# Optimization experiments

Measured on AMD Instinct MI355X. Metric: run time of the kernel, lower is better.

The kernel has to match this reference:

```python
import jax, jax.numpy as jnp
import numpy as np

CONF_THRESH = 0.01
TOP_K = 200
NMS_THRESH = 0.45


def setup_inputs() -> dict:
    key = jax.random.key(0)
    k1, k2, k3, k4, k5 = jax.random.split(key, 5)
    B, N, C = 32, 8732, 21
    return {
        "loc_data": jax.random.normal(k1, (B, N, 4), jnp.float32),
        "conf_data": jax.random.normal(k2, (B, N, C), jnp.float32),
        "pose_data": jax.random.normal(k3, (B, N, 32), jnp.float32),
        "line_data": jax.random.normal(k4, (B, N, 3), jnp.float32),
        "dbox_list": jax.random.uniform(k5, (N, 4), jnp.float32),
    }


def decode(loc, dbox):
    # loc, dbox: [N,4]; variances 0.1 / 0.2 as in the torch decode()
    cxcy = dbox[:, :2] + loc[:, :2] * 0.1 * dbox[:, 2:]
    wh = dbox[:, 2:] * jnp.exp(loc[:, 2:] * 0.2)
    mins = cxcy - wh / 2.0
    maxs = mins + wh
    return jnp.concatenate([mins, maxs], axis=1)  # [N,4] xyxy


def nms_class(boxes, scores, poses, lines):
    """Greedy NMS for one (batch, class). boxes [N,4], scores [N] (softmax probs).
    Matches torch nm_suppression: candidates are the top_k by score above
    conf_thresh; suppress IoU > overlap; at most top_k kept."""
    s0 = jnp.where(scores > CONF_THRESH, scores, -jnp.inf)
    _, cand_idx = jax.lax.top_k(s0, TOP_K)  # descending-score candidate pool
    cb = boxes[cand_idx]                     # [K,4]
    cs = s0[cand_idx]                        # [K], -inf where below threshold
    x1, y1, x2, y2 = cb[:, 0], cb[:, 1], cb[:, 2], cb[:, 3]
    area = (x2 - x1) * (y2 - y1)
    K = TOP_K
    ar = jnp.arange(K)

    def step(s, _):
        i = jnp.argmax(s)
        take = jnp.isfinite(s[i])
        xx1 = jnp.maximum(x1, x1[i])
        yy1 = jnp.maximum(y1, y1[i])
        xx2 = jnp.minimum(x2, x2[i])
        yy2 = jnp.minimum(y2, y2[i])
        inter = jnp.clip(xx2 - xx1, 0.0) * jnp.clip(yy2 - yy1, 0.0)
        union = area - inter + area[i]
        iou = inter / union
        supp = (iou > NMS_THRESH) | (ar == i)
        s_new = jnp.where(take & supp, -jnp.inf, s)
        return s_new, (i, take)

    _, (pos, take) = jax.lax.scan(step, cs, None, length=K)
    gi = cand_idx[pos]  # global box indices of kept detections [K]
    row = jnp.concatenate(
        [scores[gi][:, None], boxes[gi], poses[gi], lines[gi]], axis=1
    )  # [K, 1+4+32+3] = [200, 40]
    return row * take[:, None].astype(row.dtype)


def reference(loc_data, conf_data, pose_data, line_data, dbox_list):
    conf = jax.nn.softmax(conf_data, axis=-1)                       # [B,N,C]
    boxes = jax.vmap(decode, in_axes=(0, None))(loc_data, dbox_list)  # [B,N,4]
    per_cls = jax.vmap(nms_class, in_axes=(None, 1, None, None))    # over classes
    per_batch = jax.vmap(per_cls, in_axes=(0, 0, 0, 0))             # over batch
    out = per_batch(boxes, conf, pose_data, line_data)              # [B,C,200,40]
    return out.at[:, 0].set(0.0)  # class 0 (background) is skipped in torch loop
```

## Files before the change

### kernel.cpp

```cpp
#include <hip/hip_runtime.h>
#include <math.h>

#define BB 32
#define NN 8732
#define CC 21
#define TOPK 200
#define NPOSE 32
#define NLINE 3
#define NBINS 2048
#define CAP 1024
#define ROWW 40

__device__ __forceinline__ double fexp(double x) {
  const double LOG2E = 1.4426950408889634074;
  const double LN2HI = 6.93147180369123816490e-01;
  const double LN2LO = 1.90821492927058770002e-10;
  double kd = rint(x * LOG2E);
  double r = fma(-kd, LN2HI, x);
  r = fma(-kd, LN2LO, r);
  double p = 2.08767569878680989792e-09;
  p = fma(p, r, 2.50521083854417187751e-08);
  p = fma(p, r, 2.75573192239858906526e-07);
  p = fma(p, r, 2.75573192239858925110e-06);
  p = fma(p, r, 2.48015873015873015873e-05);
  p = fma(p, r, 1.98412698412698412698e-04);
  p = fma(p, r, 1.38888888888888888889e-03);
  p = fma(p, r, 8.33333333333333333333e-03);
  p = fma(p, r, 4.16666666666666666667e-02);
  p = fma(p, r, 1.66666666666666666667e-01);
  p = fma(p, r, 0.5);
  p = fma(p, r, 1.0);
  p = fma(p, r, 1.0);
  int k = (int)kd;
  k = k < -1020 ? -1020 : (k > 1020 ? 1020 : k);
  double sc = __longlong_as_double((long long)(1023 + k) << 52);
  return p * sc;
}

__global__ __launch_bounds__(256, 4) void score_kernel(
    const float* __restrict__ conf, float* __restrict__ scores) {
  __shared__ __align__(16) float buf[256 * CC];
  const int tid = threadIdx.x;
  const int i0 = blockIdx.x * 256;
  const int base = i0 * CC;
  int total = BB * NN * CC - base;
  if (total > 256 * CC) total = 256 * CC;
  {
    const float4* g4 = (const float4*)(conf + base);
    float4* b4 = (float4*)buf;
    const int n4 = total >> 2;
    for (int t = tid; t < n4; t += 256) b4[t] = g4[t];
  }
  __syncthreads();
  const int i = i0 + tid;
  if (i >= BB * NN) return;
  const float* p = buf + tid * CC;
  float x[CC];
#pragma unroll
  for (int c = 0; c < CC; ++c) x[c] = p[c];
  float m = x[0];
#pragma unroll
  for (int c = 1; c < CC; ++c) m = fmaxf(m, x[c]);
  float e[CC];
#pragma unroll
  for (int c = 0; c < CC; ++c) e[c] = (float)fexp((double)(x[c] - m));
  float r0 = e[0] + e[8], r1 = e[1] + e[9], r2 = e[2] + e[10], r3 = e[3] + e[11];
  float r4 = e[4] + e[12], r5 = e[5] + e[13], r6 = e[6] + e[14], r7 = e[7] + e[15];
  float sum = ((r0 + r1) + (r2 + r3)) + ((r4 + r5) + (r6 + r7));
  sum += e[16]; sum += e[17]; sum += e[18]; sum += e[19]; sum += e[20];
  const int b = i / NN, n = i - b * NN;
#pragma unroll
  for (int c = 0; c < CC; ++c)
    scores[((size_t)b * CC + c) * NN + n] = e[c] / sum;
}

__global__ __launch_bounds__(256) void aux_kernel(
    const float* __restrict__ conf, float2* __restrict__ aux) {
  int i = blockIdx.x * 256 + threadIdx.x;
  if (i >= BB * NN) return;
  const float* p = conf + (size_t)i * CC;
  float m = p[0];
#pragma unroll
  for (int c = 1; c < CC; ++c) m = fmaxf(m, p[c]);
  float e[CC];
#pragma unroll 1
  for (int c = 0; c < CC; ++c) e[c] = (float)fexp((double)(p[c] - m));
  float r0 = e[0] + e[8], r1 = e[1] + e[9], r2 = e[2] + e[10], r3 = e[3] + e[11];
  float r4 = e[4] + e[12], r5 = e[5] + e[13], r6 = e[6] + e[14], r7 = e[7] + e[15];
  float sum = ((r0 + r1) + (r2 + r3)) + ((r4 + r5) + (r6 + r7));
  sum += e[16]; sum += e[17]; sum += e[18]; sum += e[19]; sum += e[20];
  aux[i] = make_float2(m, sum);
}

__device__ __forceinline__ int score_bin(float s) {
  unsigned u = __float_as_uint(s);
  int bin = (int)(u >> 15) - 30720;
  return bin < 0 ? 0 : (bin > NBINS - 1 ? NBINS - 1 : bin);
}

__device__ __forceinline__ float score_at(int mode, int b, int c, int n,
                                          const float* conf, const float2* auxB,
                                          const float* confB) {
  if (mode == 1) {
    float2 a = auxB[n];
    return (float)fexp((double)(confB[(size_t)n * CC] - a.x)) / a.y;
  }
  const float* p = conf + ((size_t)b * NN + n) * CC;
  float mm = p[0];
  for (int c2 = 1; c2 < CC; ++c2) mm = fmaxf(mm, p[c2]);
  float e[CC];
  for (int c2 = 0; c2 < CC; ++c2) e[c2] = (float)fexp((double)(p[c2] - mm));
  float r0 = e[0] + e[8], r1 = e[1] + e[9], r2 = e[2] + e[10], r3 = e[3] + e[11];
  float r4 = e[4] + e[12], r5 = e[5] + e[13], r6 = e[6] + e[14], r7 = e[7] + e[15];
  float sum = ((r0 + r1) + (r2 + r3)) + ((r4 + r5) + (r6 + r7));
  sum += e[16]; sum += e[17]; sum += e[18]; sum += e[19]; sum += e[20];
  return e[c] / sum;
}

__global__ __launch_bounds__(256) void nms_kernel(
    const float* __restrict__ loc, const float* __restrict__ conf,
    const float* __restrict__ pose, const float* __restrict__ line,
    const float* __restrict__ dbox, const float* __restrict__ scores,
    const float2* __restrict__ aux, int mode, float* __restrict__ out) {
  const int bc = blockIdx.x;
  const int b = bc / CC, c = bc - b * CC;
  const int tid = threadIdx.x;
  const int wv = tid >> 6, lane = tid & 63;
  float* outSlab = out + (size_t)bc * (TOPK * ROWW);
  const float4 z4 = make_float4(0.f, 0.f, 0.f, 0.f);

  if (c == 0) {
    float4* o4 = (float4*)outSlab;
    for (int i = tid; i < TOPK * ROWW / 4; i += 256) o4[i] = z4;
    return;
  }

  __shared__ int hist[NBINS];
  __shared__ float cscore[CAP];
  __shared__ int cidx[CAP];
  __shared__ float bx1[TOPK], by1[TOPK], bx2[TOPK], by2[TOPK], barea[TOPK];
  __shared__ unsigned long long supp[TOPK * 4];
  __shared__ int kept[TOPK];
  __shared__ int waveTot[4];
  __shared__ int sBT, sCnt, sKept;

  for (int i = tid; i < NBINS; i += 256) hist[i] = 0;
  if (tid == 0) { sCnt = 0; sBT = 0; }
  __syncthreads();

  const float* scoresB = scores + ((size_t)b * CC + c) * NN;
  const float2* auxB = aux + (size_t)b * NN;
  const float* confB = conf + (size_t)b * NN * CC + c;

  float4 v[9];
  if (mode == 2) {
#pragma unroll
    for (int k = 0; k < 8; ++k)
      v[k] = *(const float4*)(scoresB + k * 1024 + tid * 4);
    if (tid < 135)
      v[8] = *(const float4*)(scoresB + 8192 + tid * 4);
    else
      v[8] = make_float4(-1.f, -1.f, -1.f, -1.f);
#pragma unroll
    for (int k = 0; k < 9; ++k) {
      if (v[k].x > 0.01f) atomicAdd(&hist[score_bin(v[k].x)], 1);
      if (v[k].y > 0.01f) atomicAdd(&hist[score_bin(v[k].y)], 1);
      if (v[k].z > 0.01f) atomicAdd(&hist[score_bin(v[k].z)], 1);
      if (v[k].w > 0.01f) atomicAdd(&hist[score_bin(v[k].w)], 1);
    }
  } else {
    for (int n = tid; n < NN; n += 256) {
      float s = score_at(mode, b, c, n, conf, auxB, confB);
      if (s > 0.01f) atomicAdd(&hist[score_bin(s)], 1);
    }
  }
  __syncthreads();

  int s8 = 0;
#pragma unroll
  for (int k = 0; k < 8; ++k) s8 += hist[tid * 8 + k];
  int cs = s8;
#pragma unroll
  for (int d = 1; d < 64; d <<= 1) {
    int t = __shfl_down(cs, d, 64);
    if (lane + d < 64) cs += t;
  }
  if (lane == 0) waveTot[wv] = cs;
  __syncthreads();
  {
    int higher = 0;
    for (int g = wv + 1; g < 4; ++g) higher += waveTot[g];
    int incl = cs + higher;
    int excl = incl - s8;
    if (excl < TOPK && incl >= TOPK) {
      int cum = excl, bt = tid * 8;
      for (int bin = tid * 8 + 7;; --bin) {
        cum += hist[bin];
        if (cum >= TOPK || bin == tid * 8) { bt = bin; break; }
      }
      sBT = bt;
    }
  }
  __syncthreads();
  const int bt = sBT;

  if (mode == 2) {
#pragma unroll
    for (int k = 0; k < 9; ++k) {
      float sv[4] = {v[k].x, v[k].y, v[k].z, v[k].w};
#pragma unroll
      for (int j = 0; j < 4; ++j) {
        float s = sv[j];
        if (s > 0.01f && score_bin(s) >= bt) {
          int p = atomicAdd(&sCnt, 1);
          if (p < CAP) { cscore[p] = s; cidx[p] = k * 1024 + tid * 4 + j; }
        }
      }
    }
  } else {
    for (int n = tid; n < NN; n += 256) {
      float s = score_at(mode, b, c, n, conf, auxB, confB);
      if (s > 0.01f && score_bin(s) >= bt) {
        int p = atomicAdd(&sCnt, 1);
        if (p < CAP) { cscore[p] = s; cidx[p] = n; }
      }
    }
  }
  __syncthreads();
  const int M = sCnt < CAP ? sCnt : CAP;
  if (M == 0) {
    float4* o4 = (float4*)outSlab;
    for (int i = tid; i < TOPK * ROWW / 4; i += 256) o4[i] = z4;
    return;
  }

  int P = 1;
  while (P < M) P <<= 1;
  for (int i = M + tid; i < P; i += 256) {
    cscore[i] = -1e30f;
    cidx[i] = 0x7fffffff;
  }
  __syncthreads();
  for (int k = 2; k <= P; k <<= 1) {
    for (int j = k >> 1; j > 0; j >>= 1) {
      for (int i = tid; i < P; i += 256) {
        int ixj = i ^ j;
        if (ixj > i) {
          float si = cscore[i], sj = cscore[ixj];
          int ii = cidx[i], ij = cidx[ixj];
          bool agt = (si > sj) || (si == sj && ii < ij);
          bool up = ((i & k) == 0);
          if (up ? !agt : agt) {
            cscore[i] = sj; cscore[ixj] = si;
            cidx[i] = ij;  cidx[ixj] = ii;
          }
        }
      }
      __syncthreads();
    }
  }

  const int K = M < TOPK ? M : TOPK;

  const float* locB = loc + (size_t)b * NN * 4;
  for (int t = tid; t < K; t += 256) {
    int n = cidx[t];
    float l0 = locB[(size_t)n * 4 + 0], l1 = locB[(size_t)n * 4 + 1];
    float l2 = locB[(size_t)n * 4 + 2], l3 = locB[(size_t)n * 4 + 3];
    float d0 = dbox[(size_t)n * 4 + 0], d1 = dbox[(size_t)n * 4 + 1];
    float d2 = dbox[(size_t)n * 4 + 2], d3 = dbox[(size_t)n * 4 + 3];
    float cx = d0 + (l0 * 0.1f) * d2;
    float cy = d1 + (l1 * 0.1f) * d3;
    float w = d2 * (float)fexp((double)(l2 * 0.2f));
    float h = d3 * (float)fexp((double)(l3 * 0.2f));
    float x1 = cx - w * 0.5f;
    float y1 = cy - h * 0.5f;
    float x2 = x1 + w;
    float y2 = y1 + h;
    bx1[t] = x1; by1[t] = y1; bx2[t] = x2; by2[t] = y2;
    barea[t] = (x2 - x1) * (y2 - y1);
  }
  __syncthreads();

  {
    const int l = wv * 64 + lane;
    float lx1 = 0.f, ly1 = 0.f, lx2 = 0.f, ly2 = 0.f, lar = 0.f;
    const bool lvalid = l < K;
    if (lvalid) { lx1 = bx1[l]; ly1 = by1[l]; lx2 = bx2[l]; ly2 = by2[l]; lar = barea[l]; }
    const int wtop = wv * 64 + 63;
    for (int j = 0; j < K; ++j) {
      unsigned long long mres = 0;
      if (wtop > j) {
        float jx1 = bx1[j], jy1 = by1[j], jx2 = bx2[j], jy2 = by2[j], ja = barea[j];
        float xx1 = fmaxf(lx1, jx1);
        float yy1 = fmaxf(ly1, jy1);
        float xx2 = fminf(lx2, jx2);
        float yy2 = fminf(ly2, jy2);
        float iw = fmaxf(xx2 - xx1, 0.0f);
        float ih = fmaxf(yy2 - yy1, 0.0f);
        float inter = iw * ih;
        float uni = (lar - inter) + ja;
        bool hit = lvalid & (l > j) & (inter / uni > 0.45f);
        mres = __ballot((int)hit);
      }
      if (lane == 0) supp[j * 4 + wv] = mres;
    }
  }
  __syncthreads();

  if (tid == 0) {
    unsigned long long alive[4];
#pragma unroll
    for (int w = 0; w < 4; ++w) {
      int cnt = K - w * 64;
      alive[w] = cnt <= 0 ? 0ull : (cnt >= 64 ? ~0ull : ((1ull << cnt) - 1ull));
    }
    int nk = 0;
#pragma unroll
    for (int w = 0; w < 4; ++w) {
      while (alive[w]) {
        int bit = __ffsll(alive[w]) - 1;
        int j = w * 64 + bit;
        kept[nk++] = j;
        unsigned long long r0 = supp[j * 4 + 0];
        unsigned long long r1 = supp[j * 4 + 1];
        unsigned long long r2 = supp[j * 4 + 2];
        unsigned long long r3 = supp[j * 4 + 3];
        alive[w] &= ~(1ull << bit);
        alive[0] &= ~r0; alive[1] &= ~r1; alive[2] &= ~r2; alive[3] &= ~r3;
      }
    }
    sKept = nk;
  }
  __syncthreads();

  const int nk = sKept;
  const float* poseB = pose + (size_t)b * NN * NPOSE;
  const float* lineB = line + (size_t)b * NN * NLINE;
  for (int t = tid; t < nk; t += 256) {
    int j = kept[t];
    int n = cidx[j];
    float* row = outSlab + (size_t)t * ROWW;
    row[0] = cscore[j];
    row[1] = bx1[j];
    row[2] = by1[j];
    row[3] = bx2[j];
    row[4] = by2[j];
    const float4* p4 = (const float4*)(poseB + (size_t)n * NPOSE);
#pragma unroll
    for (int q = 0; q < 8; ++q) {
      float4 pv = p4[q];
      row[5 + 4 * q + 0] = pv.x;
      row[5 + 4 * q + 1] = pv.y;
      row[5 + 4 * q + 2] = pv.z;
      row[5 + 4 * q + 3] = pv.w;
    }
    row[37] = lineB[(size_t)n * NLINE + 0];
    row[38] = lineB[(size_t)n * NLINE + 1];
    row[39] = lineB[(size_t)n * NLINE + 2];
  }
  {
    const int zq = (TOPK - nk) * 10;
    float4* o4 = (float4*)(outSlab + (size_t)nk * ROWW);
    for (int q = tid; q < zq; q += 256) o4[q] = z4;
  }
}

extern "C" void kernel_launch(void* const* d_in, const int* in_sizes, int n_in,
                              void* d_out, int out_size, void* d_ws, size_t ws_size,
                              hipStream_t stream) {
  const float* loc  = (const float*)d_in[0];
  const float* conf = (const float*)d_in[1];
  const float* pose = (const float*)d_in[2];
  const float* line = (const float*)d_in[3];
  const float* dbox = (const float*)d_in[4];
  float* out = (float*)d_out;

  const size_t scoreBytes = (size_t)BB * CC * NN * sizeof(float);
  const size_t auxBytes   = (size_t)BB * NN * sizeof(float2);

  int mode;
  float* scores = nullptr;
  float2* aux = nullptr;
  if (ws_size >= scoreBytes) {
    mode = 2; scores = (float*)d_ws;
  } else if (ws_size >= auxBytes) {
    mode = 1; aux = (float2*)d_ws;
  } else {
    mode = 0;
  }

  const int total = BB * NN;
  if (mode == 2) {
    score_kernel<<<(total + 255) / 256, 256, 0, stream>>>(conf, scores);
  } else if (mode == 1) {
    aux_kernel<<<(total + 255) / 256, 256, 0, stream>>>(conf, aux);
  }
  nms_kernel<<<BB * CC, 256, 0, stream>>>(loc, conf, pose, line, dbox,
                                          scores, aux, mode, out);
}
```

Baseline: 187.1 us.

## Replace full per-class score tensor with per-row softmax max/sum stats

The pre-pass that wrote a full transposed [B,C,N] softmax score tensor is dropped. A smem-staged kernel now writes only a per-row (max, sum) pair. The NMS kernel recomputes each class score from conf plus these stats once, keeps the scores in registers, and reuses them for both the histogram and the candidate-selection passes. The greedy NMS scan also skips reading suppression rows that are entirely zero, using a ballot-built bitmask. This cuts large workspace write/read traffic, at the cost of strided 84-byte-stride conf reads and a double-precision exp per element inside the NMS kernel.

```diff
diff --git a/kernel.cpp b/kernel.cpp
--- a/kernel.cpp
+++ b/kernel.cpp
@@ -37,8 +37,8 @@
   return p * sc;
 }
 
-__global__ __launch_bounds__(256, 4) void score_kernel(
-    const float* __restrict__ conf, float* __restrict__ scores) {
+__global__ __launch_bounds__(256) void aux_kernel(
+    const float* __restrict__ conf, float2* __restrict__ aux) {
   __shared__ __align__(16) float buf[256 * CC];
   const int tid = threadIdx.x;
   const int i0 = blockIdx.x * 256;
@@ -55,30 +55,6 @@
   const int i = i0 + tid;
   if (i >= BB * NN) return;
   const float* p = buf + tid * CC;
-  float x[CC];
-#pragma unroll
-  for (int c = 0; c < CC; ++c) x[c] = p[c];
-  float m = x[0];
-#pragma unroll
-  for (int c = 1; c < CC; ++c) m = fmaxf(m, x[c]);
-  float e[CC];
-#pragma unroll
-  for (int c = 0; c < CC; ++c) e[c] = (float)fexp((double)(x[c] - m));
-  float r0 = e[0] + e[8], r1 = e[1] + e[9], r2 = e[2] + e[10], r3 = e[3] + e[11];
-  float r4 = e[4] + e[12], r5 = e[5] + e[13], r6 = e[6] + e[14], r7 = e[7] + e[15];
-  float sum = ((r0 + r1) + (r2 + r3)) + ((r4 + r5) + (r6 + r7));
-  sum += e[16]; sum += e[17]; sum += e[18]; sum += e[19]; sum += e[20];
-  const int b = i / NN, n = i - b * NN;
-#pragma unroll
-  for (int c = 0; c < CC; ++c)
-    scores[((size_t)b * CC + c) * NN + n] = e[c] / sum;
-}
-
-__global__ __launch_bounds__(256) void aux_kernel(
-    const float* __restrict__ conf, float2* __restrict__ aux) {
-  int i = blockIdx.x * 256 + threadIdx.x;
-  if (i >= BB * NN) return;
-  const float* p = conf + (size_t)i * CC;
   float m = p[0];
 #pragma unroll
   for (int c = 1; c < CC; ++c) m = fmaxf(m, p[c]);
@@ -98,13 +74,7 @@
   return bin < 0 ? 0 : (bin > NBINS - 1 ? NBINS - 1 : bin);
 }
 
-__device__ __forceinline__ float score_at(int mode, int b, int c, int n,
-                                          const float* conf, const float2* auxB,
-                                          const float* confB) {
-  if (mode == 1) {
-    float2 a = auxB[n];
-    return (float)fexp((double)(confB[(size_t)n * CC] - a.x)) / a.y;
-  }
+__device__ __forceinline__ float score_full(const float* conf, int b, int c, int n) {
   const float* p = conf + ((size_t)b * NN + n) * CC;
   float mm = p[0];
   for (int c2 = 1; c2 < CC; ++c2) mm = fmaxf(mm, p[c2]);
@@ -120,8 +90,8 @@
 __global__ __launch_bounds__(256) void nms_kernel(
     const float* __restrict__ loc, const float* __restrict__ conf,
     const float* __restrict__ pose, const float* __restrict__ line,
-    const float* __restrict__ dbox, const float* __restrict__ scores,
-    const float2* __restrict__ aux, int mode, float* __restrict__ out) {
+    const float* __restrict__ dbox, const float2* __restrict__ aux,
+    int mode, float* __restrict__ out) {
   const int bc = blockIdx.x;
   const int b = bc / CC, c = bc - b * CC;
   const int tid = threadIdx.x;
@@ -140,6 +110,7 @@
   __shared__ int cidx[CAP];
   __shared__ float bx1[TOPK], by1[TOPK], bx2[TOPK], by2[TOPK], barea[TOPK];
   __shared__ unsigned long long supp[TOPK * 4];
+  __shared__ unsigned long long rowAnyBits[4];
   __shared__ int kept[TOPK];
   __shared__ int waveTot[4];
   __shared__ int sBT, sCnt, sKept;
@@ -148,31 +119,46 @@
   if (tid == 0) { sCnt = 0; sBT = 0; }
   __syncthreads();
 
-  const float* scoresB = scores + ((size_t)b * CC + c) * NN;
   const float2* auxB = aux + (size_t)b * NN;
   const float* confB = conf + (size_t)b * NN * CC + c;
 
-  float4 v[9];
-  if (mode == 2) {
-#pragma unroll
-    for (int k = 0; k < 8; ++k)
-      v[k] = *(const float4*)(scoresB + k * 1024 + tid * 4);
-    if (tid < 135)
-      v[8] = *(const float4*)(scoresB + 8192 + tid * 4);
-    else
-      v[8] = make_float4(-1.f, -1.f, -1.f, -1.f);
+  float s36[36];
+  if (mode == 1) {
 #pragma unroll
     for (int k = 0; k < 9; ++k) {
-      if (v[k].x > 0.01f) atomicAdd(&hist[score_bin(v[k].x)], 1);
-      if (v[k].y > 0.01f) atomicAdd(&hist[score_bin(v[k].y)], 1);
-      if (v[k].z > 0.01f) atomicAdd(&hist[score_bin(v[k].z)], 1);
-      if (v[k].w > 0.01f) atomicAdd(&hist[score_bin(v[k].w)], 1);
+      const int n0 = k * 1024 + (tid << 2);
+      if (k < 8 || tid < 135) {
+        float4 a01 = *(const float4*)(auxB + n0);
+        float4 a23 = *(const float4*)(auxB + n0 + 2);
+        float c0 = confB[(size_t)(n0 + 0) * CC];
+        float c1 = confB[(size_t)(n0 + 1) * CC];
+        float c2 = confB[(size_t)(n0 + 2) * CC];
+        float c3 = confB[(size_t)(n0 + 3) * CC];
+        s36[k * 4 + 0] = (float)fexp((double)(c0 - a01.x)) / a01.y;
+        s36[k * 4 + 1] = (float)fexp((double)(c1 - a01.z)) / a01.w;
+        s36[k * 4 + 2] = (float)fexp((double)(c2 - a23.x)) / a23.y;
+        s36[k * 4 + 3] = (float)fexp((double)(c3 - a23.z)) / a23.w;
+      } else {
+        s36[k * 4 + 0] = -1.f; s36[k * 4 + 1] = -1.f;
+        s36[k * 4 + 2] = -1.f; s36[k * 4 + 3] = -1.f;
+      }
     }
   } else {
-    for (int n = tid; n < NN; n += 256) {
-      float s = score_at(mode, b, c, n, conf, auxB, confB);
-      if (s > 0.01f) atomicAdd(&hist[score_bin(s)], 1);
-    }
+#pragma unroll 1
+    for (int k = 0; k < 9; ++k) {
+      const int n0 = k * 1024 + (tid << 2);
+      if (k < 8 || tid < 135) {
+        for (int q = 0; q < 4; ++q) s36[k * 4 + q] = score_full(conf, b, c, n0 + q);
+      } else {
+        for (int q = 0; q < 4; ++q) s36[k * 4 + q] = -1.f;
+      }
+    }
+  }
+
+#pragma unroll
+  for (int k2 = 0; k2 < 36; ++k2) {
+    float s = s36[k2];
+    if (s > 0.01f) atomicAdd(&hist[score_bin(s)], 1);
   }
   __syncthreads();
 
@@ -204,25 +190,14 @@
   __syncthreads();
   const int bt = sBT;
 
-  if (mode == 2) {
-#pragma unroll
-    for (int k = 0; k < 9; ++k) {
-      float sv[4] = {v[k].x, v[k].y, v[k].z, v[k].w};
-#pragma unroll
-      for (int j = 0; j < 4; ++j) {
-        float s = sv[j];
-        if (s > 0.01f && score_bin(s) >= bt) {
-          int p = atomicAdd(&sCnt, 1);
-          if (p < CAP) { cscore[p] = s; cidx[p] = k * 1024 + tid * 4 + j; }
-        }
-      }
-    }
-  } else {
-    for (int n = tid; n < NN; n += 256) {
-      float s = score_at(mode, b, c, n, conf, auxB, confB);
-      if (s > 0.01f && score_bin(s) >= bt) {
-        int p = atomicAdd(&sCnt, 1);
-        if (p < CAP) { cscore[p] = s; cidx[p] = n; }
+#pragma unroll
+  for (int k2 = 0; k2 < 36; ++k2) {
+    float s = s36[k2];
+    if (s > 0.01f && score_bin(s) >= bt) {
+      int p = atomicAdd(&sCnt, 1);
+      if (p < CAP) {
+        cscore[p] = s;
+        cidx[p] = (k2 >> 2) * 1024 + (tid << 2) + (k2 & 3);
       }
     }
   }
@@ -308,6 +283,16 @@
   }
   __syncthreads();
 
+  {
+    bool nz = false;
+    if (tid < K)
+      nz = (supp[tid * 4 + 0] | supp[tid * 4 + 1] |
+            supp[tid * 4 + 2] | supp[tid * 4 + 3]) != 0ull;
+    unsigned long long bal = __ballot((int)nz);
+    if (lane == 0) rowAnyBits[wv] = bal;
+  }
+  __syncthreads();
+
   if (tid == 0) {
     unsigned long long alive[4];
 #pragma unroll
@@ -318,16 +303,19 @@
     int nk = 0;
 #pragma unroll
     for (int w = 0; w < 4; ++w) {
+      const unsigned long long raw = rowAnyBits[w];
       while (alive[w]) {
         int bit = __ffsll(alive[w]) - 1;
         int j = w * 64 + bit;
         kept[nk++] = j;
-        unsigned long long r0 = supp[j * 4 + 0];
-        unsigned long long r1 = supp[j * 4 + 1];
-        unsigned long long r2 = supp[j * 4 + 2];
-        unsigned long long r3 = supp[j * 4 + 3];
         alive[w] &= ~(1ull << bit);
-        alive[0] &= ~r0; alive[1] &= ~r1; alive[2] &= ~r2; alive[3] &= ~r3;
+        if ((raw >> bit) & 1) {
+          unsigned long long r0 = supp[j * 4 + 0];
+          unsigned long long r1 = supp[j * 4 + 1];
+          unsigned long long r2 = supp[j * 4 + 2];
+          unsigned long long r3 = supp[j * 4 + 3];
+          alive[0] &= ~r0; alive[1] &= ~r1; alive[2] &= ~r2; alive[3] &= ~r3;
+        }
       }
     }
     sKept = nk;
@@ -376,26 +364,14 @@
   const float* dbox = (const float*)d_in[4];
   float* out = (float*)d_out;
 
-  const size_t scoreBytes = (size_t)BB * CC * NN * sizeof(float);
-  const size_t auxBytes   = (size_t)BB * NN * sizeof(float2);
-
-  int mode;
-  float* scores = nullptr;
-  float2* aux = nullptr;
-  if (ws_size >= scoreBytes) {
-    mode = 2; scores = (float*)d_ws;
-  } else if (ws_size >= auxBytes) {
-    mode = 1; aux = (float2*)d_ws;
-  } else {
-    mode = 0;
-  }
-
-  const int total = BB * NN;
-  if (mode == 2) {
-    score_kernel<<<(total + 255) / 256, 256, 0, stream>>>(conf, scores);
-  } else if (mode == 1) {
+  const size_t auxBytes = (size_t)BB * NN * sizeof(float2);
+  int mode = (ws_size >= auxBytes) ? 1 : 0;
+  float2* aux = mode ? (float2*)d_ws : nullptr;
+
+  if (mode) {
+    const int total = BB * NN;
     aux_kernel<<<(total + 255) / 256, 256, 0, stream>>>(conf, aux);
   }
   nms_kernel<<<BB * CC, 256, 0, stream>>>(loc, conf, pose, line, dbox,
-                                          scores, aux, mode, out);
-}
+                                          aux, mode, out);
+}
```

After: 231.3 us. 23.6% more time.

## Replace bitonic candidate sort with rank-by-count selection and skip empty suppression rows

Applied to the files above, without the earlier changes.

Packs each candidate's score and index into one 64-bit key and gives every candidate its final position by counting how many keys are larger. This replaces the bitonic sort that needed many barriers. Boxes are stored as float4 and loaded with vector loads. The IoU test becomes a double-precision FMA against a threshold, which avoids the divide. A bitmap of rows with any suppression lets the serial greedy pass skip supp reads for rows that suppress nothing. The aux-workspace fallback path is removed. The counting rank costs O(M^2) shared-memory reads, which may be slow when the candidate pool is large.

```diff
diff --git a/kernel.cpp b/kernel.cpp
--- a/kernel.cpp
+++ b/kernel.cpp
@@ -74,37 +74,13 @@
     scores[((size_t)b * CC + c) * NN + n] = e[c] / sum;
 }
 
-__global__ __launch_bounds__(256) void aux_kernel(
-    const float* __restrict__ conf, float2* __restrict__ aux) {
-  int i = blockIdx.x * 256 + threadIdx.x;
-  if (i >= BB * NN) return;
-  const float* p = conf + (size_t)i * CC;
-  float m = p[0];
-#pragma unroll
-  for (int c = 1; c < CC; ++c) m = fmaxf(m, p[c]);
-  float e[CC];
-#pragma unroll 1
-  for (int c = 0; c < CC; ++c) e[c] = (float)fexp((double)(p[c] - m));
-  float r0 = e[0] + e[8], r1 = e[1] + e[9], r2 = e[2] + e[10], r3 = e[3] + e[11];
-  float r4 = e[4] + e[12], r5 = e[5] + e[13], r6 = e[6] + e[14], r7 = e[7] + e[15];
-  float sum = ((r0 + r1) + (r2 + r3)) + ((r4 + r5) + (r6 + r7));
-  sum += e[16]; sum += e[17]; sum += e[18]; sum += e[19]; sum += e[20];
-  aux[i] = make_float2(m, sum);
-}
-
 __device__ __forceinline__ int score_bin(float s) {
   unsigned u = __float_as_uint(s);
   int bin = (int)(u >> 15) - 30720;
   return bin < 0 ? 0 : (bin > NBINS - 1 ? NBINS - 1 : bin);
 }
 
-__device__ __forceinline__ float score_at(int mode, int b, int c, int n,
-                                          const float* conf, const float2* auxB,
-                                          const float* confB) {
-  if (mode == 1) {
-    float2 a = auxB[n];
-    return (float)fexp((double)(confB[(size_t)n * CC] - a.x)) / a.y;
-  }
+__device__ __forceinline__ float score_full(const float* conf, int b, int c, int n) {
   const float* p = conf + ((size_t)b * NN + n) * CC;
   float mm = p[0];
   for (int c2 = 1; c2 < CC; ++c2) mm = fmaxf(mm, p[c2]);
@@ -121,7 +97,7 @@
     const float* __restrict__ loc, const float* __restrict__ conf,
     const float* __restrict__ pose, const float* __restrict__ line,
     const float* __restrict__ dbox, const float* __restrict__ scores,
-    const float2* __restrict__ aux, int mode, float* __restrict__ out) {
+    int mode, float* __restrict__ out) {
   const int bc = blockIdx.x;
   const int b = bc / CC, c = bc - b * CC;
   const int tid = threadIdx.x;
@@ -136,10 +112,13 @@
   }
 
   __shared__ int hist[NBINS];
-  __shared__ float cscore[CAP];
-  __shared__ int cidx[CAP];
-  __shared__ float bx1[TOPK], by1[TOPK], bx2[TOPK], by2[TOPK], barea[TOPK];
+  __shared__ unsigned long long ckey[CAP];
+  __shared__ float4 cbox[TOPK];
+  __shared__ float carea[TOPK];
+  __shared__ float sScore[TOPK];
+  __shared__ int sIdx[TOPK];
   __shared__ unsigned long long supp[TOPK * 4];
+  __shared__ unsigned long long rowAnyBits[4];
   __shared__ int kept[TOPK];
   __shared__ int waveTot[4];
   __shared__ int sBT, sCnt, sKept;
@@ -149,11 +128,9 @@
   __syncthreads();
 
   const float* scoresB = scores + ((size_t)b * CC + c) * NN;
-  const float2* auxB = aux + (size_t)b * NN;
-  const float* confB = conf + (size_t)b * NN * CC + c;
 
   float4 v[9];
-  if (mode == 2) {
+  if (mode == 1) {
 #pragma unroll
     for (int k = 0; k < 8; ++k)
       v[k] = *(const float4*)(scoresB + k * 1024 + tid * 4);
@@ -161,18 +138,27 @@
       v[8] = *(const float4*)(scoresB + 8192 + tid * 4);
     else
       v[8] = make_float4(-1.f, -1.f, -1.f, -1.f);
-#pragma unroll
+  } else {
+#pragma unroll 1
     for (int k = 0; k < 9; ++k) {
-      if (v[k].x > 0.01f) atomicAdd(&hist[score_bin(v[k].x)], 1);
-      if (v[k].y > 0.01f) atomicAdd(&hist[score_bin(v[k].y)], 1);
-      if (v[k].z > 0.01f) atomicAdd(&hist[score_bin(v[k].z)], 1);
-      if (v[k].w > 0.01f) atomicAdd(&hist[score_bin(v[k].w)], 1);
-    }
-  } else {
-    for (int n = tid; n < NN; n += 256) {
-      float s = score_at(mode, b, c, n, conf, auxB, confB);
-      if (s > 0.01f) atomicAdd(&hist[score_bin(s)], 1);
-    }
+      const int n0 = k * 1024 + (tid << 2);
+      if (k < 8 || tid < 135) {
+        v[k].x = score_full(conf, b, c, n0 + 0);
+        v[k].y = score_full(conf, b, c, n0 + 1);
+        v[k].z = score_full(conf, b, c, n0 + 2);
+        v[k].w = score_full(conf, b, c, n0 + 3);
+      } else {
+        v[k] = make_float4(-1.f, -1.f, -1.f, -1.f);
+      }
+    }
+  }
+
+#pragma unroll
+  for (int k = 0; k < 9; ++k) {
+    if (v[k].x > 0.01f) atomicAdd(&hist[score_bin(v[k].x)], 1);
+    if (v[k].y > 0.01f) atomicAdd(&hist[score_bin(v[k].y)], 1);
+    if (v[k].z > 0.01f) atomicAdd(&hist[score_bin(v[k].z)], 1);
+    if (v[k].w > 0.01f) atomicAdd(&hist[score_bin(v[k].w)], 1);
   }
   __syncthreads();
 
@@ -204,25 +190,19 @@
   __syncthreads();
   const int bt = sBT;
 
-  if (mode == 2) {
-#pragma unroll
-    for (int k = 0; k < 9; ++k) {
-      float sv[4] = {v[k].x, v[k].y, v[k].z, v[k].w};
-#pragma unroll
-      for (int j = 0; j < 4; ++j) {
-        float s = sv[j];
-        if (s > 0.01f && score_bin(s) >= bt) {
-          int p = atomicAdd(&sCnt, 1);
-          if (p < CAP) { cscore[p] = s; cidx[p] = k * 1024 + tid * 4 + j; }
-        }
-      }
-    }
-  } else {
-    for (int n = tid; n < NN; n += 256) {
-      float s = score_at(mode, b, c, n, conf, auxB, confB);
+#pragma unroll
+  for (int k = 0; k < 9; ++k) {
+    float sv[4] = {v[k].x, v[k].y, v[k].z, v[k].w};
+#pragma unroll
+    for (int j = 0; j < 4; ++j) {
+      float s = sv[j];
       if (s > 0.01f && score_bin(s) >= bt) {
         int p = atomicAdd(&sCnt, 1);
-        if (p < CAP) { cscore[p] = s; cidx[p] = n; }
+        if (p < CAP) {
+          unsigned n = (unsigned)(k * 1024 + (tid << 2) + j);
+          ckey[p] = ((unsigned long long)__float_as_uint(s) << 32) |
+                    (unsigned long long)(0xFFFFFFFFu - n);
+        }
       }
     }
   }
@@ -233,78 +213,72 @@
     for (int i = tid; i < TOPK * ROWW / 4; i += 256) o4[i] = z4;
     return;
   }
-
-  int P = 1;
-  while (P < M) P <<= 1;
-  for (int i = M + tid; i < P; i += 256) {
-    cscore[i] = -1e30f;
-    cidx[i] = 0x7fffffff;
-  }
-  __syncthreads();
-  for (int k = 2; k <= P; k <<= 1) {
-    for (int j = k >> 1; j > 0; j >>= 1) {
-      for (int i = tid; i < P; i += 256) {
-        int ixj = i ^ j;
-        if (ixj > i) {
-          float si = cscore[i], sj = cscore[ixj];
-          int ii = cidx[i], ij = cidx[ixj];
-          bool agt = (si > sj) || (si == sj && ii < ij);
-          bool up = ((i & k) == 0);
-          if (up ? !agt : agt) {
-            cscore[i] = sj; cscore[ixj] = si;
-            cidx[i] = ij;  cidx[ixj] = ii;
-          }
-        }
-      }
-      __syncthreads();
-    }
-  }
-
   const int K = M < TOPK ? M : TOPK;
 
+  for (int t = tid; t < M; t += 256) {
+    unsigned long long kt = ckey[t];
+    int r = 0;
+    for (int j = 0; j < M; ++j) r += (ckey[j] > kt) ? 1 : 0;
+    if (r < TOPK) {
+      sScore[r] = __uint_as_float((unsigned)(kt >> 32));
+      sIdx[r] = (int)(0xFFFFFFFFu - (unsigned)(kt & 0xFFFFFFFFull));
+    }
+  }
+  __syncthreads();
+
   const float* locB = loc + (size_t)b * NN * 4;
-  for (int t = tid; t < K; t += 256) {
-    int n = cidx[t];
-    float l0 = locB[(size_t)n * 4 + 0], l1 = locB[(size_t)n * 4 + 1];
-    float l2 = locB[(size_t)n * 4 + 2], l3 = locB[(size_t)n * 4 + 3];
-    float d0 = dbox[(size_t)n * 4 + 0], d1 = dbox[(size_t)n * 4 + 1];
-    float d2 = dbox[(size_t)n * 4 + 2], d3 = dbox[(size_t)n * 4 + 3];
-    float cx = d0 + (l0 * 0.1f) * d2;
-    float cy = d1 + (l1 * 0.1f) * d3;
-    float w = d2 * (float)fexp((double)(l2 * 0.2f));
-    float h = d3 * (float)fexp((double)(l3 * 0.2f));
+  if (tid < K) {
+    int n = sIdx[tid];
+    float4 l4 = *(const float4*)(locB + (size_t)n * 4);
+    float4 d4 = *(const float4*)(dbox + (size_t)n * 4);
+    float cx = d4.x + (l4.x * 0.1f) * d4.z;
+    float cy = d4.y + (l4.y * 0.1f) * d4.w;
+    float w = d4.z * (float)fexp((double)(l4.z * 0.2f));
+    float h = d4.w * (float)fexp((double)(l4.w * 0.2f));
     float x1 = cx - w * 0.5f;
     float y1 = cy - h * 0.5f;
     float x2 = x1 + w;
     float y2 = y1 + h;
-    bx1[t] = x1; by1[t] = y1; bx2[t] = x2; by2[t] = y2;
-    barea[t] = (x2 - x1) * (y2 - y1);
-  }
-  __syncthreads();
-
-  {
+    cbox[tid] = make_float4(x1, y1, x2, y2);
+    carea[tid] = (x2 - x1) * (y2 - y1);
+  }
+  __syncthreads();
+
+  {
+    const double TMID = (double)0.45f + 0x1p-26;
     const int l = wv * 64 + lane;
-    float lx1 = 0.f, ly1 = 0.f, lx2 = 0.f, ly2 = 0.f, lar = 0.f;
     const bool lvalid = l < K;
-    if (lvalid) { lx1 = bx1[l]; ly1 = by1[l]; lx2 = bx2[l]; ly2 = by2[l]; lar = barea[l]; }
-    const int wtop = wv * 64 + 63;
-    for (int j = 0; j < K; ++j) {
-      unsigned long long mres = 0;
-      if (wtop > j) {
-        float jx1 = bx1[j], jy1 = by1[j], jx2 = bx2[j], jy2 = by2[j], ja = barea[j];
-        float xx1 = fmaxf(lx1, jx1);
-        float yy1 = fmaxf(ly1, jy1);
-        float xx2 = fminf(lx2, jx2);
-        float yy2 = fminf(ly2, jy2);
-        float iw = fmaxf(xx2 - xx1, 0.0f);
-        float ih = fmaxf(yy2 - yy1, 0.0f);
-        float inter = iw * ih;
-        float uni = (lar - inter) + ja;
-        bool hit = lvalid & (l > j) & (inter / uni > 0.45f);
-        mres = __ballot((int)hit);
-      }
+    float4 lb = lvalid ? cbox[l] : z4;
+    float lar = lvalid ? carea[l] : 0.f;
+    const int jlim = (K < wv * 64 + 63) ? K : (wv * 64 + 63);
+    for (int j = 0; j < jlim; ++j) {
+      float4 jb = cbox[j];
+      float ja = carea[j];
+      float xx1 = fmaxf(lb.x, jb.x);
+      float yy1 = fmaxf(lb.y, jb.y);
+      float xx2 = fminf(lb.z, jb.z);
+      float yy2 = fminf(lb.w, jb.w);
+      float iw = fmaxf(xx2 - xx1, 0.0f);
+      float ih = fmaxf(yy2 - yy1, 0.0f);
+      float inter = iw * ih;
+      float uni = (lar - inter) + ja;
+      double tt = fma(-TMID, (double)uni, (double)inter);
+      bool hit = lvalid & (l > j) & (tt > 0.0);
+      unsigned long long mres = __ballot((int)hit);
       if (lane == 0) supp[j * 4 + wv] = mres;
     }
+    if (lane == 0)
+      for (int j = jlim; j < K; ++j) supp[j * 4 + wv] = 0ull;
+  }
+  __syncthreads();
+
+  {
+    bool nz = false;
+    if (tid < K)
+      nz = (supp[tid * 4 + 0] | supp[tid * 4 + 1] |
+            supp[tid * 4 + 2] | supp[tid * 4 + 3]) != 0ull;
+    unsigned long long bal = __ballot((int)nz);
+    if (lane == 0) rowAnyBits[wv] = bal;
   }
   __syncthreads();
 
@@ -318,16 +292,19 @@
     int nk = 0;
 #pragma unroll
     for (int w = 0; w < 4; ++w) {
+      const unsigned long long raw = rowAnyBits[w];
       while (alive[w]) {
         int bit = __ffsll(alive[w]) - 1;
         int j = w * 64 + bit;
         kept[nk++] = j;
-        unsigned long long r0 = supp[j * 4 + 0];
-        unsigned long long r1 = supp[j * 4 + 1];
-        unsigned long long r2 = supp[j * 4 + 2];
-        unsigned long long r3 = supp[j * 4 + 3];
         alive[w] &= ~(1ull << bit);
-        alive[0] &= ~r0; alive[1] &= ~r1; alive[2] &= ~r2; alive[3] &= ~r3;
+        if ((raw >> bit) & 1) {
+          unsigned long long r0 = supp[j * 4 + 0];
+          unsigned long long r1 = supp[j * 4 + 1];
+          unsigned long long r2 = supp[j * 4 + 2];
+          unsigned long long r3 = supp[j * 4 + 3];
+          alive[0] &= ~r0; alive[1] &= ~r1; alive[2] &= ~r2; alive[3] &= ~r3;
+        }
       }
     }
     sKept = nk;
@@ -339,13 +316,14 @@
   const float* lineB = line + (size_t)b * NN * NLINE;
   for (int t = tid; t < nk; t += 256) {
     int j = kept[t];
-    int n = cidx[j];
+    int n = sIdx[j];
     float* row = outSlab + (size_t)t * ROWW;
-    row[0] = cscore[j];
-    row[1] = bx1[j];
-    row[2] = by1[j];
-    row[3] = bx2[j];
-    row[4] = by2[j];
+    float4 bx = cbox[j];
+    row[0] = sScore[j];
+    row[1] = bx.x;
+    row[2] = bx.y;
+    row[3] = bx.z;
+    row[4] = bx.w;
     const float4* p4 = (const float4*)(poseB + (size_t)n * NPOSE);
 #pragma unroll
     for (int q = 0; q < 8; ++q) {
@@ -377,25 +355,13 @@
   float* out = (float*)d_out;
 
   const size_t scoreBytes = (size_t)BB * CC * NN * sizeof(float);
-  const size_t auxBytes   = (size_t)BB * NN * sizeof(float2);
-
-  int mode;
-  float* scores = nullptr;
-  float2* aux = nullptr;
-  if (ws_size >= scoreBytes) {
-    mode = 2; scores = (float*)d_ws;
-  } else if (ws_size >= auxBytes) {
-    mode = 1; aux = (float2*)d_ws;
-  } else {
-    mode = 0;
-  }
-
-  const int total = BB * NN;
-  if (mode == 2) {
+  int mode = (ws_size >= scoreBytes) ? 1 : 0;
+  float* scores = mode ? (float*)d_ws : nullptr;
+
+  if (mode) {
+    const int total = BB * NN;
     score_kernel<<<(total + 255) / 256, 256, 0, stream>>>(conf, scores);
-  } else if (mode == 1) {
-    aux_kernel<<<(total + 255) / 256, 256, 0, stream>>>(conf, aux);
   }
   nms_kernel<<<BB * CC, 256, 0, stream>>>(loc, conf, pose, line, dbox,
-                                          scores, aux, mode, out);
-}
+                                          scores, mode, out);
+}
```

Result: slower. 194.1 us (+3.7%).
